# Kernel tuning notes

Hardware: AMD Instinct MI355X
Metric: run time of the kernel (lower is better)

The kernel has to match this reference:

```python
import jax, jax.numpy as jnp
import numpy as np
import math

B, S, E = 2, 2048, 1024
H, HD = 16, 64  # num_heads, head_size


def setup_inputs() -> dict:
    key = jax.random.key(0)
    ks = jax.random.split(key, 9)
    sc = 1.0 / math.sqrt(HD)
    return {
        "x": jax.random.normal(ks[0], (B, S, E), dtype=jnp.float32),
        "Wq_w": jax.random.normal(ks[1], (HD, HD), dtype=jnp.float32) * sc,
        "Wq_b": jax.random.normal(ks[2], (HD,), dtype=jnp.float32) * 0.02,
        "Wk_w": jax.random.normal(ks[3], (HD, HD), dtype=jnp.float32) * sc,
        "Wk_b": jax.random.normal(ks[4], (HD,), dtype=jnp.float32) * 0.02,
        "Wv_w": jax.random.normal(ks[5], (HD, HD), dtype=jnp.float32) * sc,
        "Wv_b": jax.random.normal(ks[6], (HD,), dtype=jnp.float32) * 0.02,
        "proj_w": jax.random.normal(ks[7], (E, E), dtype=jnp.float32) * (1.0 / math.sqrt(E)),
        "proj_b": jax.random.normal(ks[8], (E,), dtype=jnp.float32) * 0.02,
    }


def reference(x, Wq_w, Wq_b, Wk_w, Wk_b, Wv_w, Wv_b, proj_w, proj_b):
    b, s, _ = x.shape
    xh = x.reshape(b, s, H, HD)  # split heads; QKV linears act per-head (shared weights)
    # torch Linear: y = x @ W.T + b
    q = jnp.einsum('bshd,ed->bhse', xh, Wq_w) + Wq_b  # [B,H,S,HD]
    k = jnp.einsum('bshd,ed->bhse', xh, Wk_w) + Wk_b
    v = jnp.einsum('bshd,ed->bhse', xh, Wv_w) + Wv_b
    scores = jnp.einsum('bhqd,bhkd->bhqk', q, k) / math.sqrt(HD)
    causal = jnp.tril(jnp.ones((s, s), dtype=bool))
    scores = jnp.where(causal, scores, jnp.float32(-1e20))
    attn = jax.nn.softmax(scores, axis=-1)  # attn_dropout p=0 (eval)
    out = jnp.einsum('bhqk,bhkd->bqhd', attn, v).reshape(b, s, H * HD)
    out = out @ proj_w.T + proj_b  # resid_dropout p=0 (eval)
    return out
```

## Files before the change

kernel.cpp:

```cpp
#include <hip/hip_runtime.h>
#include <hip/hip_bf16.h>

#define B_ 2
#define S_ 2048
#define E_ 1024
#define H_ 16
#define HD_ 64
#define T_ (B_ * S_)

typedef short bf16x8 __attribute__((ext_vector_type(8)));
typedef short bf16x4 __attribute__((ext_vector_type(4)));
typedef float f32x4 __attribute__((ext_vector_type(4)));

__device__ __forceinline__ short f2bf(float f) {
  union { float f; unsigned u; } v;
  v.f = f;
  unsigned r = v.u + 0x7fffu + ((v.u >> 16) & 1u);
  return (short)(r >> 16);
}


__global__ __launch_bounds__(256) void qkv_conv_kernel(
    const float* __restrict__ x,
    const float* __restrict__ wq, const float* __restrict__ bq,
    const float* __restrict__ wk, const float* __restrict__ bk,
    const float* __restrict__ wv, const float* __restrict__ bv,
    short* __restrict__ Q, short* __restrict__ KV,
    const float* __restrict__ pw, short* __restrict__ pwb) {
  const int tid = threadIdx.x;
  if (blockIdx.x >= 512) {
    int i = ((blockIdx.x - 512) * 256 + tid) * 4;
    float4 f = *(const float4*)(pw + i);
    bf16x4 o;
    o[0] = f2bf(f.x); o[1] = f2bf(f.y); o[2] = f2bf(f.z); o[3] = f2bf(f.w);
    *(bf16x4*)(pwb + i) = o;
    return;
  }
  __shared__ short Xs[64][136];
  __shared__ short Ws[192][72];
  __shared__ short Qt[64][68], Kt[64][68], Vt[64][68];

  const int bid = blockIdx.x;
  const int tb = bid >> 3, hg = bid & 7;
  const int s0 = (tb * 64) & (S_ - 1);
  const int kt = s0 >> 6;
  const int bb = (tb * 64) >> 11;
  const int wave = tid >> 6, lane = tid & 63;
  const int lrow = lane & 15, quad = lane >> 4;

#pragma unroll
  for (int i = 0; i < 8; i++) {
    int c = tid + 256 * i;
    int row = c >> 5, col4 = c & 31;
    float4 f = *(const float4*)(x + ((long)(tb * 64 + row)) * E_ + hg * 128 + col4 * 4);
    bf16x4 o;
    o[0] = f2bf(f.x); o[1] = f2bf(f.y); o[2] = f2bf(f.z); o[3] = f2bf(f.w);
    *(bf16x4*)&Xs[row][col4 * 4] = o;
  }
#pragma unroll
  for (int m = 0; m < 3; m++) {
    const float* w = (m == 0) ? wq : (m == 1) ? wk : wv;
#pragma unroll
    for (int i = 0; i < 4; i++) {
      int c = tid + 256 * i;
      int row = m * 64 + (c >> 4), col = (c & 15) * 4;
      float4 f = *(const float4*)(w + (long)c * 4);
      bf16x4 o;
      o[0] = f2bf(f.x); o[1] = f2bf(f.y); o[2] = f2bf(f.z); o[3] = f2bf(f.w);
      *(bf16x4*)&Ws[row][col] = o;
    }
  }
  float bias[12];
#pragma unroll
  for (int nb = 0; nb < 12; nb++) {
    int sel = nb >> 2;
    int e = ((nb & 3) * 16) + lrow;
    bias[nb] = ((sel == 0) ? bq : (sel == 1) ? bk : bv)[e];
  }
  __syncthreads();

  bf16x8 bf0[12], bf1[12];
#pragma unroll
  for (int nb = 0; nb < 12; nb++) {
    bf0[nb] = *(bf16x8*)&Ws[nb * 16 + lrow][quad * 8];
    bf1[nb] = *(bf16x8*)&Ws[nb * 16 + lrow][32 + quad * 8];
  }

  const float QSCALE = 0.125f * 1.44269504089f;
  for (int hl = 0; hl < 2; hl++) {
    const int h = hg * 2 + hl;
    bf16x8 a0 = *(bf16x8*)&Xs[wave * 16 + lrow][hl * 64 + quad * 8];
    bf16x8 a1 = *(bf16x8*)&Xs[wave * 16 + lrow][hl * 64 + 32 + quad * 8];
#pragma unroll
    for (int nb = 0; nb < 12; nb++) {
      f32x4 acc = {0.f, 0.f, 0.f, 0.f};
      acc = __builtin_amdgcn_mfma_f32_16x16x32_bf16(a0, bf0[nb], acc, 0, 0, 0);
      acc = __builtin_amdgcn_mfma_f32_16x16x32_bf16(a1, bf1[nb], acc, 0, 0, 0);
      const int sel = nb >> 2;
      const float scale = (sel == 0) ? QSCALE : 1.0f;
      short (*ct)[68] = (sel == 0) ? Qt : (sel == 1) ? Kt : Vt;
#pragma unroll
      for (int r = 0; r < 4; r++) {
        ct[wave * 16 + quad * 4 + r][(nb & 3) * 16 + lrow] =
            f2bf((acc[r] + bias[nb]) * scale);
      }
    }
    __syncthreads();

    const int bh = bb * H_ + h;
    short* Qg = Q + ((long)bh * S_ + s0) * HD_;
    short* Tg = KV + ((long)(bh * 32 + kt)) * 8192;
#pragma unroll
    for (int i = 0; i < 2; i++) {
      int c = tid + 256 * i;
      int row = c >> 3, col = (c & 7) * 8;
      *(bf16x8*)(Qg + (long)row * HD_ + col) = *(bf16x8*)&Qt[row][col];
    }
#pragma unroll
    for (int u = 0; u < 4; u++) {
      int fid = tid + 256 * u;
      bf16x8 val;
      int lane2 = fid & 63;
      int quad2 = lane2 >> 4, lrow2 = lane2 & 15;
      if (u < 2) {
        int g = fid >> 6;
        int nb = g >> 1, half = g & 1;
        val = *(bf16x8*)&Kt[nb * 16 + lrow2][half * 32 + quad2 * 8];
      } else {
        int g = (fid >> 6) & 7;
        int p2 = g >> 2, db = g & 3;
#pragma unroll
        for (int j = 0; j < 8; j++) {
          int key = (2 * p2 + (j >> 2)) * 16 + quad2 * 4 + (j & 3);
          val[j] = Vt[key][db * 16 + lrow2];
        }
      }
      *(bf16x8*)(Tg + fid * 8) = val;
    }
    __syncthreads();
  }
}

__global__ __launch_bounds__(256) void attn_kernel(
    const short* __restrict__ Q, const short* __restrict__ KV,
    short* __restrict__ O ) {
  __shared__ short L[2][8192];

  const int tid = threadIdx.x;
  const int bid = blockIdx.x;
  const int bh = bid & 31;
  const int pr = bid >> 5;
  const int b = bh >> 4, h = bh & 15;
  const long qbase = ((long)bh) << 17;

  const int wave = tid >> 6, lane = tid & 63;
  const int lrow = lane & 15, quad = lane >> 4;

  const short* Tg = KV + ((long)bh * 32) * 8192 + tid * 8;

  bf16x8 reg[4];
  auto LD = [&](int kt) {
    const short* p = Tg + (long)kt * 8192;
#pragma unroll
    for (int u = 0; u < 4; u++) reg[u] = *(const bf16x8*)(p + u * 2048);
  };

  const int qts[2] = {pr, 31 - pr};
  LD(0);
  int it = 0;
  for (int ph = 0; ph < 2; ph++) {
    const int qt = qts[ph];
    const int q0w = qt * 64 + wave * 16;
    const int qg = q0w + lrow;
    const short* qp = Q + qbase + (long)qg * HD_;
    bf16x8 qf0 = *(const bf16x8*)(qp + quad * 8);
    bf16x8 qf1 = *(const bf16x8*)(qp + 32 + quad * 8);

    f32x4 Oacc[4];
#pragma unroll
    for (int db = 0; db < 4; db++) Oacc[db] = f32x4{0.f, 0.f, 0.f, 0.f};
    float lsum = 0.f;

    const int nkt = qt + 1;
    for (int kt = 0; kt < nkt; kt++, it++) {
      const int buf = it & 1;
#pragma unroll
      for (int u = 0; u < 4; u++)
        *(bf16x8*)&L[buf][(tid + 256 * u) * 8] = reg[u];
      __syncthreads();

      {
        int ktn = kt + 1;
        bool have = true;
        if (ktn == nkt) {
          if (ph == 0) ktn = 0; else have = false;
        }
        if (have) LD(ktn);
      }

      f32x4 sc[4];
#pragma unroll
      for (int nb = 0; nb < 4; nb++) {
        bf16x8 ka0 = *(bf16x8*)&L[buf][(nb * 2 + 0) * 512 + lane * 8];
        bf16x8 ka1 = *(bf16x8*)&L[buf][(nb * 2 + 1) * 512 + lane * 8];
        f32x4 acc = {0.f, 0.f, 0.f, 0.f};
        acc = __builtin_amdgcn_mfma_f32_16x16x32_bf16(ka0, qf0, acc, 0, 0, 0);
        acc = __builtin_amdgcn_mfma_f32_16x16x32_bf16(ka1, qf1, acc, 0, 0, 0);
        sc[nb] = acc;
      }

      if (kt == qt) {
        const int k0 = kt * 64;
#pragma unroll
        for (int nb = 0; nb < 4; nb++) {
          int kgl = k0 + nb * 16 + quad * 4;
#pragma unroll
          for (int r = 0; r < 4; r++)
            if (kgl + r > qg) sc[nb][r] = -1e30f;
        }
      }

      bf16x4 pf[4];
#pragma unroll
      for (int nb = 0; nb < 4; nb++) {
        unsigned u[4];
#pragma unroll
        for (int r = 0; r < 4; r++) {
          float p = __builtin_amdgcn_exp2f(sc[nb][r]);
          lsum += p;
          u[r] = __float_as_uint(p) + 0x8000u;
        }
        unsigned lo = __builtin_amdgcn_perm(u[1], u[0], 0x07060302u);
        unsigned hi = __builtin_amdgcn_perm(u[3], u[2], 0x07060302u);
        union { unsigned q[2]; bf16x4 v; } pk;
        pk.q[0] = lo; pk.q[1] = hi;
        pf[nb] = pk.v;
      }

#pragma unroll
      for (int p2 = 0; p2 < 2; p2++) {
#pragma unroll
        for (int db = 0; db < 4; db++) {
          bf16x8 vv = *(bf16x8*)&L[buf][4096 + (p2 * 4 + db) * 512 + lane * 8];
          bf16x4 vlo = {vv[0], vv[1], vv[2], vv[3]};
          bf16x4 vhi = {vv[4], vv[5], vv[6], vv[7]};
          Oacc[db] = __builtin_amdgcn_mfma_f32_16x16x16bf16_1k(vlo, pf[2 * p2], Oacc[db], 0, 0, 0);
          Oacc[db] = __builtin_amdgcn_mfma_f32_16x16x16bf16_1k(vhi, pf[2 * p2 + 1], Oacc[db], 0, 0, 0);
        }
      }
    }

    lsum += __shfl_xor(lsum, 16);
    lsum += __shfl_xor(lsum, 32);
    const float invl = 1.f / lsum;
    const long token = (long)b * S_ + qg;
    short* obase = O + token * E_ + h * HD_;
#pragma unroll
    for (int db = 0; db < 4; db++) {
      bf16x4 o;
#pragma unroll
      for (int r = 0; r < 4; r++) o[r] = f2bf(Oacc[db][r] * invl);
      *(bf16x4*)(obase + db * 16 + quad * 4) = o;
    }
  }
}

__global__ __launch_bounds__(256) void proj_kernel(
    const short* __restrict__ A, const short* __restrict__ W,
    const float* __restrict__ bias, float* __restrict__ out) {
  __shared__ short As[2][128][40];
  __shared__ short Bs[2][64][40];
  const int tid = threadIdx.x;
  const int bid = blockIdx.x;
  const int m0 = (bid >> 4) * 128;
  const int n0 = (bid & 15) * 64;
  const int wave = tid >> 6, lane = tid & 63;
  const int wm = wave >> 1, wn = wave & 1;
  const int lrow = lane & 15, quad = lane >> 4;

  const int ar = tid >> 1, ac = (tid & 1) * 16;
  const int br = tid >> 2, bc = (tid & 3) * 8;

  bf16x8 a0, a1, b0;
  auto LDR = [&](int k0) {
    const short* ap = A + (long)(m0 + ar) * E_ + k0 + ac;
    a0 = *(const bf16x8*)(ap);
    a1 = *(const bf16x8*)(ap + 8);
    b0 = *(const bf16x8*)(W + (long)(n0 + br) * E_ + k0 + bc);
  };

  f32x4 acc[4][2];
#pragma unroll
  for (int i = 0; i < 4; i++)
#pragma unroll
    for (int j = 0; j < 2; j++) acc[i][j] = f32x4{0.f, 0.f, 0.f, 0.f};

  LDR(0);
  for (int kk = 0; kk < 32; kk++) {
    const int buf = kk & 1;
    *(bf16x8*)&As[buf][ar][ac] = a0;
    *(bf16x8*)&As[buf][ar][ac + 8] = a1;
    *(bf16x8*)&Bs[buf][br][bc] = b0;
    __syncthreads();
    if (kk < 31) LDR((kk + 1) * 32);

    bf16x8 af[4], bfr[2];
#pragma unroll
    for (int i = 0; i < 4; i++)
      af[i] = *(bf16x8*)&As[buf][wm * 64 + i * 16 + lrow][quad * 8];
#pragma unroll
    for (int j = 0; j < 2; j++)
      bfr[j] = *(bf16x8*)&Bs[buf][wn * 32 + j * 16 + lrow][quad * 8];
#pragma unroll
    for (int i = 0; i < 4; i++)
#pragma unroll
      for (int j = 0; j < 2; j++)
        acc[i][j] = __builtin_amdgcn_mfma_f32_16x16x32_bf16(af[i], bfr[j], acc[i][j], 0, 0, 0);
  }

#pragma unroll
  for (int j = 0; j < 2; j++) {
    int col = n0 + wn * 32 + j * 16 + lrow;
    float bv = bias[col];
#pragma unroll
    for (int i = 0; i < 4; i++) {
#pragma unroll
      for (int r = 0; r < 4; r++) {
        int row = m0 + wm * 64 + i * 16 + quad * 4 + r;
        out[(long)row * E_ + col] = acc[i][j][r] + bv;
      }
    }
  }
}

extern "C" void kernel_launch(void* const* d_in, const int* in_sizes, int n_in,
                              void* d_out, int out_size, void* d_ws, size_t ws_size,
                              hipStream_t stream) {
  const float* x  = (const float*)d_in[0];
  const float* wq = (const float*)d_in[1];
  const float* bq = (const float*)d_in[2];
  const float* wk = (const float*)d_in[3];
  const float* bk = (const float*)d_in[4];
  const float* wv = (const float*)d_in[5];
  const float* bv = (const float*)d_in[6];
  const float* pw = (const float*)d_in[7];
  const float* pb = (const float*)d_in[8];
  float* out = (float*)d_out;

  char* ws = (char*)d_ws;
  short* Qb = (short*)(ws);
  short* KVb = (short*)(ws + (size_t)8 * 1024 * 1024);
  short* AO = (short*)(ws + (size_t)24 * 1024 * 1024);
  short* PW = (short*)(ws + (size_t)32 * 1024 * 1024);

  qkv_conv_kernel<<<dim3(512 + 1024), dim3(256), 0, stream>>>(
      x, wq, bq, wk, bk, wv, bv, Qb, KVb, pw, PW);
  attn_kernel<<<dim3(16 * 32), dim3(256), 0, stream>>>(Qb, KVb, AO);
  proj_kernel<<<dim3(32 * 16), dim3(256), 0, stream>>>(AO, PW, pb, out);
}
```

Before: 146.6 us.

## Drop LDS staging in attention; read K/V fragments directly from global

The attention kernel no longer stages K/V tiles through shared memory with double buffering and barriers. Each wave now loads its MFMA K and V fragments straight from global memory, relying on caches for reuse across the four waves. It also drops the paired query-tile scheme, launching one block per query tile (1024 blocks), heaviest tiles first, instead of 512 blocks each taking a short and a long tile. This removes LDS traffic and __syncthreads, but every wave now issues its own global loads, which raises L2 traffic and exposes load latency that is no longer prefetched.

```diff
diff --git a/kernel.cpp b/kernel.cpp
--- a/kernel.cpp
+++ b/kernel.cpp
@@ -144,124 +144,102 @@
 __global__ __launch_bounds__(256) void attn_kernel(
     const short* __restrict__ Q, const short* __restrict__ KV,
     short* __restrict__ O ) {
-  __shared__ short L[2][8192];
-
   const int tid = threadIdx.x;
   const int bid = blockIdx.x;
   const int bh = bid & 31;
-  const int pr = bid >> 5;
+  const int g = 31 - (bid >> 5);
   const int b = bh >> 4, h = bh & 15;
   const long qbase = ((long)bh) << 17;
 
   const int wave = tid >> 6, lane = tid & 63;
   const int lrow = lane & 15, quad = lane >> 4;
-
-  const short* Tg = KV + ((long)bh * 32) * 8192 + tid * 8;
-
-  bf16x8 reg[4];
-  auto LD = [&](int kt) {
-    const short* p = Tg + (long)kt * 8192;
-#pragma unroll
-    for (int u = 0; u < 4; u++) reg[u] = *(const bf16x8*)(p + u * 2048);
-  };
-
-  const int qts[2] = {pr, 31 - pr};
-  LD(0);
-  int it = 0;
-  for (int ph = 0; ph < 2; ph++) {
-    const int qt = qts[ph];
-    const int q0w = qt * 64 + wave * 16;
-    const int qg = q0w + lrow;
-    const short* qp = Q + qbase + (long)qg * HD_;
-    bf16x8 qf0 = *(const bf16x8*)(qp + quad * 8);
-    bf16x8 qf1 = *(const bf16x8*)(qp + 32 + quad * 8);
-
-    f32x4 Oacc[4];
-#pragma unroll
-    for (int db = 0; db < 4; db++) Oacc[db] = f32x4{0.f, 0.f, 0.f, 0.f};
-    float lsum = 0.f;
-
-    const int nkt = qt + 1;
-    for (int kt = 0; kt < nkt; kt++, it++) {
-      const int buf = it & 1;
-#pragma unroll
-      for (int u = 0; u < 4; u++)
-        *(bf16x8*)&L[buf][(tid + 256 * u) * 8] = reg[u];
-      __syncthreads();
-
-      {
-        int ktn = kt + 1;
-        bool have = true;
-        if (ktn == nkt) {
-          if (ph == 0) ktn = 0; else have = false;
-        }
-        if (have) LD(ktn);
-      }
-
-      f32x4 sc[4];
+  const int qs = 4 * g + wave;
+  const int qg = qs * 16 + lrow;
+
+  const short* qp = Q + qbase + (long)qg * HD_;
+  bf16x8 qf0 = *(const bf16x8*)(qp + quad * 8);
+  bf16x8 qf1 = *(const bf16x8*)(qp + 32 + quad * 8);
+
+  const short* tb = KV + ((long)bh * 32) * 8192 + lane * 8;
+
+  f32x4 Oacc[4];
+#pragma unroll
+  for (int db = 0; db < 4; db++) Oacc[db] = f32x4{0.f, 0.f, 0.f, 0.f};
+  float lsum = 0.f;
+
+  const int nkt = g + 1;
+  for (int kt = 0; kt < nkt; kt++) {
+    const short* tp = tb + (long)kt * 8192;
+
+    bf16x8 kf[8];
+#pragma unroll
+    for (int g2 = 0; g2 < 8; g2++) kf[g2] = *(const bf16x8*)(tp + g2 * 512);
+
+    f32x4 sc[4];
+#pragma unroll
+    for (int nb = 0; nb < 4; nb++) {
+      f32x4 acc = {0.f, 0.f, 0.f, 0.f};
+      acc = __builtin_amdgcn_mfma_f32_16x16x32_bf16(kf[2 * nb], qf0, acc, 0, 0, 0);
+      acc = __builtin_amdgcn_mfma_f32_16x16x32_bf16(kf[2 * nb + 1], qf1, acc, 0, 0, 0);
+      sc[nb] = acc;
+    }
+
+    bf16x8 vf[8];
+#pragma unroll
+    for (int g2 = 0; g2 < 8; g2++) vf[g2] = *(const bf16x8*)(tp + 4096 + g2 * 512);
+
+    if (kt == nkt - 1) {
+      const int k0 = kt * 64;
 #pragma unroll
       for (int nb = 0; nb < 4; nb++) {
-        bf16x8 ka0 = *(bf16x8*)&L[buf][(nb * 2 + 0) * 512 + lane * 8];
-        bf16x8 ka1 = *(bf16x8*)&L[buf][(nb * 2 + 1) * 512 + lane * 8];
-        f32x4 acc = {0.f, 0.f, 0.f, 0.f};
-        acc = __builtin_amdgcn_mfma_f32_16x16x32_bf16(ka0, qf0, acc, 0, 0, 0);
-        acc = __builtin_amdgcn_mfma_f32_16x16x32_bf16(ka1, qf1, acc, 0, 0, 0);
-        sc[nb] = acc;
-      }
-
-      if (kt == qt) {
-        const int k0 = kt * 64;
-#pragma unroll
-        for (int nb = 0; nb < 4; nb++) {
-          int kgl = k0 + nb * 16 + quad * 4;
-#pragma unroll
-          for (int r = 0; r < 4; r++)
-            if (kgl + r > qg) sc[nb][r] = -1e30f;
-        }
-      }
-
-      bf16x4 pf[4];
-#pragma unroll
-      for (int nb = 0; nb < 4; nb++) {
-        unsigned u[4];
-#pragma unroll
-        for (int r = 0; r < 4; r++) {
-          float p = __builtin_amdgcn_exp2f(sc[nb][r]);
-          lsum += p;
-          u[r] = __float_as_uint(p) + 0x8000u;
-        }
-        unsigned lo = __builtin_amdgcn_perm(u[1], u[0], 0x07060302u);
-        unsigned hi = __builtin_amdgcn_perm(u[3], u[2], 0x07060302u);
-        union { unsigned q[2]; bf16x4 v; } pk;
-        pk.q[0] = lo; pk.q[1] = hi;
-        pf[nb] = pk.v;
-      }
-
-#pragma unroll
-      for (int p2 = 0; p2 < 2; p2++) {
-#pragma unroll
-        for (int db = 0; db < 4; db++) {
-          bf16x8 vv = *(bf16x8*)&L[buf][4096 + (p2 * 4 + db) * 512 + lane * 8];
-          bf16x4 vlo = {vv[0], vv[1], vv[2], vv[3]};
-          bf16x4 vhi = {vv[4], vv[5], vv[6], vv[7]};
-          Oacc[db] = __builtin_amdgcn_mfma_f32_16x16x16bf16_1k(vlo, pf[2 * p2], Oacc[db], 0, 0, 0);
-          Oacc[db] = __builtin_amdgcn_mfma_f32_16x16x16bf16_1k(vhi, pf[2 * p2 + 1], Oacc[db], 0, 0, 0);
-        }
-      }
-    }
-
-    lsum += __shfl_xor(lsum, 16);
-    lsum += __shfl_xor(lsum, 32);
-    const float invl = 1.f / lsum;
-    const long token = (long)b * S_ + qg;
-    short* obase = O + token * E_ + h * HD_;
-#pragma unroll
-    for (int db = 0; db < 4; db++) {
-      bf16x4 o;
-#pragma unroll
-      for (int r = 0; r < 4; r++) o[r] = f2bf(Oacc[db][r] * invl);
-      *(bf16x4*)(obase + db * 16 + quad * 4) = o;
-    }
+        int kgl = k0 + nb * 16 + quad * 4;
+#pragma unroll
+        for (int r = 0; r < 4; r++)
+          if (kgl + r > qg) sc[nb][r] = -1e30f;
+      }
+    }
+
+    bf16x4 pf[4];
+#pragma unroll
+    for (int nb = 0; nb < 4; nb++) {
+      unsigned u[4];
+#pragma unroll
+      for (int r = 0; r < 4; r++) {
+        float p = __builtin_amdgcn_exp2f(sc[nb][r]);
+        lsum += p;
+        u[r] = __float_as_uint(p) + 0x8000u;
+      }
+      unsigned lo = __builtin_amdgcn_perm(u[1], u[0], 0x07060302u);
+      unsigned hi = __builtin_amdgcn_perm(u[3], u[2], 0x07060302u);
+      union { unsigned q[2]; bf16x4 v; } pk;
+      pk.q[0] = lo; pk.q[1] = hi;
+      pf[nb] = pk.v;
+    }
+
+#pragma unroll
+    for (int p2 = 0; p2 < 2; p2++) {
+#pragma unroll
+      for (int db = 0; db < 4; db++) {
+        bf16x8 vv = vf[p2 * 4 + db];
+        bf16x4 vlo = {vv[0], vv[1], vv[2], vv[3]};
+        bf16x4 vhi = {vv[4], vv[5], vv[6], vv[7]};
+        Oacc[db] = __builtin_amdgcn_mfma_f32_16x16x16bf16_1k(vlo, pf[2 * p2], Oacc[db], 0, 0, 0);
+        Oacc[db] = __builtin_amdgcn_mfma_f32_16x16x16bf16_1k(vhi, pf[2 * p2 + 1], Oacc[db], 0, 0, 0);
+      }
+    }
+  }
+
+  lsum += __shfl_xor(lsum, 16);
+  lsum += __shfl_xor(lsum, 32);
+  const float invl = 1.f / lsum;
+  const long token = (long)b * S_ + qg;
+  short* obase = O + token * E_ + h * HD_;
+#pragma unroll
+  for (int db = 0; db < 4; db++) {
+    bf16x4 o;
+#pragma unroll
+    for (int r = 0; r < 4; r++) o[r] = f2bf(Oacc[db][r] * invl);
+    *(bf16x4*)(obase + db * 16 + quad * 4) = o;
   }
 }
 
@@ -355,6 +333,6 @@
 
   qkv_conv_kernel<<<dim3(512 + 1024), dim3(256), 0, stream>>>(
       x, wq, bq, wk, bk, wv, bv, Qb, KVb, pw, PW);
-  attn_kernel<<<dim3(16 * 32), dim3(256), 0, stream>>>(Qb, KVb, AO);
+  attn_kernel<<<dim3(32 * 32), dim3(256), 0, stream>>>(Qb, KVb, AO);
   proj_kernel<<<dim3(32 * 16), dim3(256), 0, stream>>>(AO, PW, pb, out);
 }
```

After: 152.3 us. +3.9%, slower.
